# Kernel tuning notes

Measured on AMD Instinct MI355X. Metric: run time of the kernel, lower is better.

## Reference

```python
import jax, jax.numpy as jnp
import numpy as np

N = 50000      # nodes
E = 800000     # edges (before self loops)
IN = 128       # in_channels
HID = 64       # hidden_channels
HEADS = 4
NCLS = 2
NEG_SLOPE = 0.2
BN_EPS = 1e-5

# per-layer config: (in_dim, heads, out_c, concat)
LAYERS = [(IN, HEADS, HID, True), (HID*HEADS, HEADS, HID, True), (HID*HEADS, HEADS, HID, True), (HID*HEADS, 1, HID, False)]

def setup_inputs():
    key = jax.random.key(0)
    ks = iter(jax.random.split(key, 64))
    d = {}
    d['x'] = jax.random.normal(next(ks), (N, IN), dtype=jnp.float32)
    d['edge_index'] = jax.random.randint(next(ks), (2, E), 0, N, dtype=jnp.int64)
    for i, (inc, h, oc, concat) in enumerate(LAYERS):
        d[f'W{i}'] = jax.random.normal(next(ks), (inc, h*oc), dtype=jnp.float32) * (1.0/np.sqrt(inc))
        d[f'as{i}'] = jax.random.normal(next(ks), (h, oc), dtype=jnp.float32) * 0.1
        d[f'ad{i}'] = jax.random.normal(next(ks), (h, oc), dtype=jnp.float32) * 0.1
        bn_dim = h*oc if concat else oc
        d[f'b{i}'] = jnp.zeros((bn_dim,), dtype=jnp.float32)
        d[f'g{i}'] = jnp.ones((bn_dim,), dtype=jnp.float32)
        d[f'be{i}'] = jnp.zeros((bn_dim,), dtype=jnp.float32)
    d['hw1'] = jax.random.normal(next(ks), (HID, HID//2), dtype=jnp.float32) * (1.0/np.sqrt(HID))
    d['hb1'] = jnp.zeros((HID//2,), dtype=jnp.float32)
    d['hw2'] = jax.random.normal(next(ks), (HID//2, NCLS), dtype=jnp.float32) * (1.0/np.sqrt(HID//2))
    d['hb2'] = jnp.zeros((NCLS,), dtype=jnp.float32)
    return d

def _gat_layer(x, src, dst, W, a_src, a_dst, bias, heads, out_c, concat):
    n = x.shape[0]
    h = (x @ W).reshape(n, heads, out_c)                 # [N,H,C]
    asrc = jnp.einsum('nhc,hc->nh', h, a_src)            # [N,H]
    adst = jnp.einsum('nhc,hc->nh', h, a_dst)            # [N,H]
    e = asrc[src] + adst[dst]                            # [Etot,H]
    e = jax.nn.leaky_relu(e, NEG_SLOPE)
    # segment softmax over incoming edges of each dst node
    m = jax.ops.segment_max(e, dst, num_segments=n)
    m = jnp.where(jnp.isfinite(m), m, 0.0)
    ex = jnp.exp(e - m[dst])
    s = jax.ops.segment_sum(ex, dst, num_segments=n)
    alpha = ex / (s[dst] + 1e-16)                        # [Etot,H]
    msg = h[src] * alpha[:, :, None]                     # [Etot,H,C]
    out = jax.ops.segment_sum(msg, dst, num_segments=n)  # [N,H,C]
    out = out.reshape(n, heads*out_c) if concat else out.mean(axis=1)
    return out + bias

def _bn(x, g, b):
    mu = x.mean(axis=0)
    var = x.var(axis=0)
    return g * (x - mu) * jax.lax.rsqrt(var + BN_EPS) + b

def reference(x, edge_index,
              W0, as0, ad0, b0, g0, be0,
              W1, as1, ad1, b1, g1, be1,
              W2, as2, ad2, b2, g2, be2,
              W3, as3, ad3, b3, g3, be3,
              hw1, hb1, hw2, hb2):
    loop = jnp.arange(N, dtype=edge_index.dtype)
    src = jnp.concatenate([edge_index[0], loop])
    dst = jnp.concatenate([edge_index[1], loop])
    params = [(W0, as0, ad0, b0, g0, be0), (W1, as1, ad1, b1, g1, be1),
              (W2, as2, ad2, b2, g2, be2), (W3, as3, ad3, b3, g3, be3)]
    h = x
    for (inc, heads, oc, concat), (W, a_s, a_d, b, g, be) in zip(LAYERS, params):
        h = _gat_layer(h, src, dst, W, a_s, a_d, b, heads, oc, concat)
        h = _bn(h, g, be)
        h = jax.nn.relu(h)
    h = jax.nn.relu(h @ hw1 + hb1)
    return h @ hw2 + hb2
```

## Files before the change

### kernel.cpp

```cpp
#include <hip/hip_runtime.h>

typedef __attribute__((ext_vector_type(8))) short bf16x8;
typedef __attribute__((ext_vector_type(4))) float f32x4;

__device__ __forceinline__ float bf2f(unsigned short u) {
    union { unsigned int i; float f; } x;
    x.i = ((unsigned int)u) << 16;
    return x.f;
}
__device__ __forceinline__ unsigned short f2bf(float f) {
    union { float f; unsigned int i; } x;
    x.f = f;
    unsigned int r = x.i + 0x7fffu + ((x.i >> 16) & 1u);
    return (unsigned short)(r >> 16);
}
__device__ __forceinline__ float ldf(const void* p, int i, int f32m) {
    if (f32m) return ((const float*)p)[i];
    return bf2f(((const unsigned short*)p)[i]);
}
__device__ __forceinline__ void unpack2(unsigned int u, float& lo, float& hi) {
    union { unsigned int i; float f; } a, b;
    a.i = u << 16;
    b.i = u & 0xffff0000u;
    lo = a.f;
    hi = b.f;
}

__global__ void zero_kernel(int* p, int n) {
    int i = blockIdx.x * 256 + threadIdx.x;
    if (i < n) p[i] = 0;
}

__global__ void probe_kernel(const int* ei, const unsigned int* xw, int* meta) {
    if (threadIdx.x == 0 && blockIdx.x == 0) {
        int orv = 0;
        for (int k = 0; k < 64; k++) orv |= ei[2 * k + 1];
        meta[0] = (orv == 0) ? 1 : 0;
        int cnt = 0;
        for (int k = 0; k < 64; k++) {
            unsigned int w = xw[k];
            int e = (int)((w >> 23) & 0xffu);
            if (e >= 107 && e <= 140) cnt++;
        }
        meta[1] = (cnt >= 48) ? 1 : 0;
    }
}

__global__ void hist_kernel(const int* ei, const int* meta, int* cnt, int E, int N) {
    int e = blockIdx.x * 256 + threadIdx.x;
    if (e >= E) return;
    int d = meta[0] ? ei[2 * (E + e)] : ei[E + e];
    if ((unsigned)d >= (unsigned)N) d = 0;
    atomicAdd(&cnt[d], 1);
}

__global__ void __launch_bounds__(256) chunkred_kernel(const int* cnt, int* csum, int N) {
    __shared__ int red[256];
    int t = threadIdx.x;
    int idx = blockIdx.x * 256 + t;
    red[t] = (idx < N) ? cnt[idx] : 0;
    __syncthreads();
    for (int off = 128; off > 0; off >>= 1) {
        if (t < off) red[t] += red[t + off];
        __syncthreads();
    }
    if (t == 0) csum[blockIdx.x] = red[0];
}

__global__ void __launch_bounds__(256) scanc_kernel(const int* csum, int* cbase, int* offs,
                                                    int nch, int N) {
    __shared__ int part[256];
    int t = threadIdx.x;
    int v = (t < nch) ? csum[t] : 0;
    part[t] = v;
    __syncthreads();
    for (int off = 1; off < 256; off <<= 1) {
        int tv = (t >= off) ? part[t - off] : 0;
        __syncthreads();
        part[t] += tv;
        __syncthreads();
    }
    if (t < nch) cbase[t] = part[t] - v;
    if (t == nch - 1) offs[N] = part[t];
}

__global__ void __launch_bounds__(256) offs_kernel(const int* cnt, const int* cbase,
                                                   int* offs, int N) {
    __shared__ int part[256];
    int t = threadIdx.x;
    int idx = blockIdx.x * 256 + t;
    int v = (idx < N) ? cnt[idx] : 0;
    part[t] = v;
    __syncthreads();
    for (int off = 1; off < 256; off <<= 1) {
        int tv = (t >= off) ? part[t - off] : 0;
        __syncthreads();
        part[t] += tv;
        __syncthreads();
    }
    if (idx < N) offs[idx] = cbase[blockIdx.x] + part[t] - v;
}

__global__ void scatter_kernel(const int* ei, const int* meta, const int* offs,
                               int* fill, int* csr, int E, int N) {
    int e = blockIdx.x * 256 + threadIdx.x;
    if (e >= E) return;
    int is64 = meta[0];
    int sv = is64 ? ei[2 * e] : ei[e];
    int d  = is64 ? ei[2 * (E + e)] : ei[E + e];
    if ((unsigned)sv >= (unsigned)N) sv = 0;
    if ((unsigned)d  >= (unsigned)N) d  = 0;
    int pos = offs[d] + atomicAdd(&fill[d], 1);
    csr[pos] = sv;
}

__global__ void __launch_bounds__(256) split_kernel(const void* X, int x_is_input,
                                                    const int* meta, const float* scale,
                                                    const float* shift, int apply_bn,
                                                    unsigned short* hi, unsigned short* lo,
                                                    int total4, int kmask) {
    int idx = blockIdx.x * 256 + threadIdx.x;
    if (idx >= total4) return;
    int base = idx * 4;
    int xmode = x_is_input ? meta[1] : 1;
    float v[4];
    if (xmode) {
        float4 f = *(const float4*)((const float*)X + base);
        v[0] = f.x; v[1] = f.y; v[2] = f.z; v[3] = f.w;
    } else {
        uint2 u = *(const uint2*)((const unsigned short*)X + base);
        unpack2(u.x, v[0], v[1]);
        unpack2(u.y, v[2], v[3]);
    }
    if (apply_bn) {
        int f0 = base & kmask;
        #pragma unroll
        for (int j = 0; j < 4; j++)
            v[j] = fmaxf(fmaf(v[j], scale[f0 + j], shift[f0 + j]), 0.0f);
    }
    unsigned short h[4], l[4];
    #pragma unroll
    for (int j = 0; j < 4; j++) {
        h[j] = f2bf(v[j]);
        l[j] = f2bf(v[j] - bf2f(h[j]));
    }
    uint2 ho, loo;
    ho.x = (unsigned int)h[0] | ((unsigned int)h[1] << 16);
    ho.y = (unsigned int)h[2] | ((unsigned int)h[3] << 16);
    loo.x = (unsigned int)l[0] | ((unsigned int)l[1] << 16);
    loo.y = (unsigned int)l[2] | ((unsigned int)l[3] << 16);
    *(uint2*)(hi + base) = ho;
    *(uint2*)(lo + base) = loo;
}

__global__ void __launch_bounds__(256) wsplit_all(const void* W0, const void* W1,
                                                  const void* W2, const void* W3,
                                                  const int* meta,
                                                  unsigned short* h0, unsigned short* l0,
                                                  unsigned short* h1, unsigned short* l1,
                                                  unsigned short* h2, unsigned short* l2,
                                                  unsigned short* h3, unsigned short* l3) {
    int e = blockIdx.x * 256 + threadIdx.x;
    const void* W;
    unsigned short *hi, *lo;
    int K, shift, idx;
    if (e < 32768)       { W = W0; hi = h0; lo = l0; K = 128; shift = 8; idx = e; }
    else if (e < 98304)  { W = W1; hi = h1; lo = l1; K = 256; shift = 8; idx = e - 32768; }
    else if (e < 163840) { W = W2; hi = h2; lo = l2; K = 256; shift = 8; idx = e - 98304; }
    else if (e < 180224) { W = W3; hi = h3; lo = l3; K = 256; shift = 6; idx = e - 163840; }
    else return;
    int k = idx >> shift;
    int n = idx & ((1 << shift) - 1);
    float x = ldf(W, idx, meta[1]);
    unsigned short h = f2bf(x);
    hi[n * K + k] = h;
    lo[n * K + k] = f2bf(x - bf2f(h));
}

__global__ void __launch_bounds__(256) gemm_mfma(const unsigned short* Ahi,
                                                 const unsigned short* Alo,
                                                 const unsigned short* Bhi,
                                                 const unsigned short* Blo,
                                                 void* Cout, int out_bf16,
                                                 const void* aw_s, const void* aw_d,
                                                 float* asrc, float* adst,
                                                 int M, int K, int NC, const int* meta) {
    __shared__ unsigned short sAhi[64 * 40];
    __shared__ unsigned short sAlo[64 * 40];
    __shared__ unsigned short sBhi[64 * 40];
    __shared__ unsigned short sBlo[64 * 40];
    int wmode = meta[1];
    int t = threadIdx.x;
    int wid = t >> 6;
    int lane = t & 63;
    int row0 = blockIdx.x * 64;
    int col0 = blockIdx.y * 64;
    int H = NC >> 6;

    int ar = t >> 2;
    int ak = (t & 3) * 8;

    f32x4 acc[4];
    #pragma unroll
    for (int i = 0; i < 4; i++) acc[i] = (f32x4){0.0f, 0.0f, 0.0f, 0.0f};

    int m = lane & 15;
    int q = lane >> 4;

    for (int kt = 0; kt < K; kt += 32) {
        {
            int gr = row0 + ar;
            uint4 h4 = {0, 0, 0, 0}, l4 = {0, 0, 0, 0};
            if (gr < M) {
                h4 = *(const uint4*)(Ahi + (size_t)gr * K + kt + ak);
                l4 = *(const uint4*)(Alo + (size_t)gr * K + kt + ak);
            }
            *(uint4*)(sAhi + ar * 40 + ak) = h4;
            *(uint4*)(sAlo + ar * 40 + ak) = l4;
            uint4 bh4 = *(const uint4*)(Bhi + (size_t)(col0 + ar) * K + kt + ak);
            uint4 bl4 = *(const uint4*)(Blo + (size_t)(col0 + ar) * K + kt + ak);
            *(uint4*)(sBhi + ar * 40 + ak) = bh4;
            *(uint4*)(sBlo + ar * 40 + ak) = bl4;
        }
        __syncthreads();

        bf16x8 ahi = *(const bf16x8*)(sAhi + (wid * 16 + m) * 40 + q * 8);
        bf16x8 alo = *(const bf16x8*)(sAlo + (wid * 16 + m) * 40 + q * 8);
        #pragma unroll
        for (int tn = 0; tn < 4; tn++) {
            bf16x8 bhi = *(const bf16x8*)(sBhi + (tn * 16 + m) * 40 + q * 8);
            bf16x8 blo = *(const bf16x8*)(sBlo + (tn * 16 + m) * 40 + q * 8);
            acc[tn] = __builtin_amdgcn_mfma_f32_16x16x32_bf16(ahi, bhi, acc[tn], 0, 0, 0);
            acc[tn] = __builtin_amdgcn_mfma_f32_16x16x32_bf16(alo, bhi, acc[tn], 0, 0, 0);
            acc[tn] = __builtin_amdgcn_mfma_f32_16x16x32_bf16(ahi, blo, acc[tn], 0, 0, 0);
        }
        __syncthreads();
    }

    #pragma unroll
    for (int tn = 0; tn < 4; tn++) {
        int gcol = col0 + tn * 16 + m;
        #pragma unroll
        for (int reg = 0; reg < 4; reg++) {
            int grow = row0 + wid * 16 + q * 4 + reg;
            if (grow < M) {
                if (out_bf16)
                    ((unsigned short*)Cout)[(size_t)grow * NC + gcol] = f2bf(acc[tn][reg]);
                else
                    ((float*)Cout)[(size_t)grow * NC + gcol] = acc[tn][reg];
            }
        }
    }

    float ps[4] = {0.f, 0.f, 0.f, 0.f};
    float pd[4] = {0.f, 0.f, 0.f, 0.f};
    #pragma unroll
    for (int tn = 0; tn < 4; tn++) {
        float asv = ldf(aw_s, blockIdx.y * 64 + tn * 16 + m, wmode);
        float adv = ldf(aw_d, blockIdx.y * 64 + tn * 16 + m, wmode);
        #pragma unroll
        for (int reg = 0; reg < 4; reg++) {
            ps[reg] = fmaf(acc[tn][reg], asv, ps[reg]);
            pd[reg] = fmaf(acc[tn][reg], adv, pd[reg]);
        }
    }
    #pragma unroll
    for (int reg = 0; reg < 4; reg++) {
        #pragma unroll
        for (int off = 1; off < 16; off <<= 1) {
            ps[reg] += __shfl_xor(ps[reg], off);
            pd[reg] += __shfl_xor(pd[reg], off);
        }
    }
    if (m == 0) {
        #pragma unroll
        for (int reg = 0; reg < 4; reg++) {
            int grow = row0 + wid * 16 + q * 4 + reg;
            if (grow < M) {
                asrc[grow * H + blockIdx.y] = ps[reg];
                adst[grow * H + blockIdx.y] = pd[reg];
            }
        }
    }
}

__global__ void __launch_bounds__(256) aggb4(const unsigned short* hfb, const float* asrc,
                                             const float* adst, const int* offs,
                                             const int* csr, float* out, int N) {
    int wid = threadIdx.x >> 6;
    int l = threadIdx.x & 63;
    int node = blockIdx.x * 4 + wid;
    if (node >= N) return;
    int h = l >> 4;
    int beg = offs[node], end = offs[node + 1];
    float ad = adst[node * 4 + h];
    float e0 = asrc[node * 4 + h] + ad;
    e0 = (e0 < 0.0f) ? 0.2f * e0 : e0;
    float w0 = __expf(e0);
    uint2 u0 = ((const uint2*)(hfb + (size_t)node * 256))[l];
    float g0a, g0b, g0c, g0d;
    unpack2(u0.x, g0a, g0b);
    unpack2(u0.y, g0c, g0d);
    float s = w0;
    float a0 = w0 * g0a, a1 = w0 * g0b, a2 = w0 * g0c, a3 = w0 * g0d;
    int i = beg;
    for (; i + 4 <= end; i += 4) {
        int s0 = csr[i], s1 = csr[i + 1], s2 = csr[i + 2], s3 = csr[i + 3];
        float e_0 = asrc[s0 * 4 + h] + ad;
        float e_1 = asrc[s1 * 4 + h] + ad;
        float e_2 = asrc[s2 * 4 + h] + ad;
        float e_3 = asrc[s3 * 4 + h] + ad;
        uint2 u_0 = ((const uint2*)(hfb + (size_t)s0 * 256))[l];
        uint2 u_1 = ((const uint2*)(hfb + (size_t)s1 * 256))[l];
        uint2 u_2 = ((const uint2*)(hfb + (size_t)s2 * 256))[l];
        uint2 u_3 = ((const uint2*)(hfb + (size_t)s3 * 256))[l];
        e_0 = (e_0 < 0.0f) ? 0.2f * e_0 : e_0;
        e_1 = (e_1 < 0.0f) ? 0.2f * e_1 : e_1;
        e_2 = (e_2 < 0.0f) ? 0.2f * e_2 : e_2;
        e_3 = (e_3 < 0.0f) ? 0.2f * e_3 : e_3;
        float wv0 = __expf(e_0), wv1 = __expf(e_1), wv2 = __expf(e_2), wv3 = __expf(e_3);
        s += (wv0 + wv1) + (wv2 + wv3);
        float x0, x1, x2, x3;
        unpack2(u_0.x, x0, x1); unpack2(u_0.y, x2, x3);
        a0 = fmaf(wv0, x0, a0); a1 = fmaf(wv0, x1, a1);
        a2 = fmaf(wv0, x2, a2); a3 = fmaf(wv0, x3, a3);
        unpack2(u_1.x, x0, x1); unpack2(u_1.y, x2, x3);
        a0 = fmaf(wv1, x0, a0); a1 = fmaf(wv1, x1, a1);
        a2 = fmaf(wv1, x2, a2); a3 = fmaf(wv1, x3, a3);
        unpack2(u_2.x, x0, x1); unpack2(u_2.y, x2, x3);
        a0 = fmaf(wv2, x0, a0); a1 = fmaf(wv2, x1, a1);
        a2 = fmaf(wv2, x2, a2); a3 = fmaf(wv2, x3, a3);
        unpack2(u_3.x, x0, x1); unpack2(u_3.y, x2, x3);
        a0 = fmaf(wv3, x0, a0); a1 = fmaf(wv3, x1, a1);
        a2 = fmaf(wv3, x2, a2); a3 = fmaf(wv3, x3, a3);
    }
    for (; i < end; i++) {
        int sn = csr[i];
        float es = asrc[sn * 4 + h] + ad;
        es = (es < 0.0f) ? 0.2f * es : es;
        float wv = __expf(es);
        uint2 u = ((const uint2*)(hfb + (size_t)sn * 256))[l];
        float x0, x1, x2, x3;
        unpack2(u.x, x0, x1); unpack2(u.y, x2, x3);
        s += wv;
        a0 = fmaf(wv, x0, a0); a1 = fmaf(wv, x1, a1);
        a2 = fmaf(wv, x2, a2); a3 = fmaf(wv, x3, a3);
    }
    float rs = 1.0f / (s + 1e-16f);
    float4 o;
    o.x = a0 * rs; o.y = a1 * rs; o.z = a2 * rs; o.w = a3 * rs;
    *(float4*)&out[(size_t)node * 256 + l * 4] = o;
}

__global__ void __launch_bounds__(256) aggf1(const float* hf, const float* asrc,
                                             const float* adst, const int* offs,
                                             const int* csr, float* out, int N) {
    int wid = threadIdx.x >> 6;
    int c = threadIdx.x & 63;
    int node = blockIdx.x * 4 + wid;
    if (node >= N) return;
    int beg = offs[node], end = offs[node + 1];
    float ad = adst[node];
    float e0 = asrc[node] + ad;
    e0 = (e0 < 0.0f) ? 0.2f * e0 : e0;
    float w0 = __expf(e0);
    float s = w0;
    float acc0 = w0 * hf[(size_t)node * 64 + c];
    float acc1 = 0.0f, acc2 = 0.0f, acc3 = 0.0f;
    int i = beg;
    for (; i + 4 <= end; i += 4) {
        int s0 = csr[i], s1 = csr[i + 1], s2 = csr[i + 2], s3 = csr[i + 3];
        float e_0 = asrc[s0] + ad;
        float e_1 = asrc[s1] + ad;
        float e_2 = asrc[s2] + ad;
        float e_3 = asrc[s3] + ad;
        float g0 = hf[(size_t)s0 * 64 + c];
        float g1 = hf[(size_t)s1 * 64 + c];
        float g2 = hf[(size_t)s2 * 64 + c];
        float g3 = hf[(size_t)s3 * 64 + c];
        e_0 = (e_0 < 0.0f) ? 0.2f * e_0 : e_0;
        e_1 = (e_1 < 0.0f) ? 0.2f * e_1 : e_1;
        e_2 = (e_2 < 0.0f) ? 0.2f * e_2 : e_2;
        e_3 = (e_3 < 0.0f) ? 0.2f * e_3 : e_3;
        float w0_ = __expf(e_0), w1_ = __expf(e_1), w2_ = __expf(e_2), w3_ = __expf(e_3);
        s += (w0_ + w1_) + (w2_ + w3_);
        acc0 = fmaf(w0_, g0, acc0);
        acc1 = fmaf(w1_, g1, acc1);
        acc2 = fmaf(w2_, g2, acc2);
        acc3 = fmaf(w3_, g3, acc3);
    }
    for (; i < end; i++) {
        int sn = csr[i];
        float es = asrc[sn] + ad;
        es = (es < 0.0f) ? 0.2f * es : es;
        float wv = __expf(es);
        s += wv;
        acc0 = fmaf(wv, hf[(size_t)sn * 64 + c], acc0);
    }
    float acc = (acc0 + acc1) + (acc2 + acc3);
    out[(size_t)node * 64 + c] = acc / (s + 1e-16f);
}

__global__ void __launch_bounds__(256) bnstats_kernel(const float* x, float* partial,
                                                      int N, int NC, int c4shift) {
    __shared__ float4 ls[256];
    __shared__ float4 lq[256];
    int t = threadIdx.x;
    int c4 = t & ((1 << c4shift) - 1);
    int rsub = t >> c4shift;
    int rstep = 256 >> c4shift;
    int r0 = blockIdx.x * 256 + rsub;
    int r1 = blockIdx.x * 256 + 256;
    if (r1 > N) r1 = N;
    float4 s = {0.f, 0.f, 0.f, 0.f}, q = {0.f, 0.f, 0.f, 0.f};
    for (int r = r0; r < r1; r += rstep) {
        float4 v = *(const float4*)(x + (size_t)r * NC + c4 * 4);
        s.x += v.x; s.y += v.y; s.z += v.z; s.w += v.w;
        q.x = fmaf(v.x, v.x, q.x);
        q.y = fmaf(v.y, v.y, q.y);
        q.z = fmaf(v.z, v.z, q.z);
        q.w = fmaf(v.w, v.w, q.w);
    }
    ls[t] = s;
    lq[t] = q;
    __syncthreads();
    for (int step = 128; step >= (1 << c4shift); step >>= 1) {
        if (t < step) {
            float4 a = ls[t + step], b = lq[t + step];
            ls[t].x += a.x; ls[t].y += a.y; ls[t].z += a.z; ls[t].w += a.w;
            lq[t].x += b.x; lq[t].y += b.y; lq[t].z += b.z; lq[t].w += b.w;
        }
        __syncthreads();
    }
    if (t < (1 << c4shift)) {
        *(float4*)(partial + (size_t)blockIdx.x * 2 * NC + t * 4) = ls[t];
        *(float4*)(partial + (size_t)blockIdx.x * 2 * NC + NC + t * 4) = lq[t];
    }
}

__global__ void bnfinal(const float* partial, int nch, const void* g, const void* be,
                        float* scale, float* shift, int NC, float invN, const int* meta) {
    int f = threadIdx.x;
    if (f >= NC) return;
    int wmode = meta[1];
    float s = 0.0f, q = 0.0f;
    for (int b = 0; b < nch; b++) {
        s += partial[(size_t)b * 2 * NC + f];
        q += partial[(size_t)b * 2 * NC + NC + f];
    }
    float mu = s * invN;
    float var = q * invN - mu * mu;
    if (var < 0.0f) var = 0.0f;
    float rs = rsqrtf(var + 1e-5f);
    float sc = ldf(g, f, wmode) * rs;
    scale[f] = sc;
    shift[f] = ldf(be, f, wmode) - mu * sc;
}

__global__ void __launch_bounds__(256) head_kernel(const float* xin, const float* bnscale,
                                                   const float* bnshift, const void* hw1,
                                                   const void* hb1, const void* hw2,
                                                   const void* hb2, void* out, int N,
                                                   const int* meta) {
    __shared__ float w1[64 * 32];
    __shared__ float w2[64];
    __shared__ float b1[32];
    __shared__ float b2[2];
    __shared__ float sc[64];
    __shared__ float sh[64];
    int wmode = meta[1];
    for (int i = threadIdx.x; i < 2048; i += 256) w1[i] = ldf(hw1, i, wmode);
    if (threadIdx.x < 64) {
        w2[threadIdx.x] = ldf(hw2, threadIdx.x, wmode);
        sc[threadIdx.x] = bnscale[threadIdx.x];
        sh[threadIdx.x] = bnshift[threadIdx.x];
    }
    if (threadIdx.x < 32) b1[threadIdx.x] = ldf(hb1, threadIdx.x, wmode);
    if (threadIdx.x < 2) b2[threadIdx.x] = ldf(hb2, threadIdx.x, wmode);
    __syncthreads();
    int n = blockIdx.x * 256 + threadIdx.x;
    if (n >= N) return;
    float x[64];
    for (int i = 0; i < 64; i++)
        x[i] = fmaxf(fmaf(xin[(size_t)n * 64 + i], sc[i], sh[i]), 0.0f);
    float o0 = b2[0], o1 = b2[1];
    for (int j = 0; j < 32; j++) {
        float a = b1[j];
        #pragma unroll
        for (int k = 0; k < 64; k++) a = fmaf(x[k], w1[k * 32 + j], a);
        a = fmaxf(a, 0.0f);
        o0 = fmaf(a, w2[j * 2], o0);
        o1 = fmaf(a, w2[j * 2 + 1], o1);
    }
    if (wmode) {
        ((float*)out)[n * 2] = o0;
        ((float*)out)[n * 2 + 1] = o1;
    } else {
        ((unsigned short*)out)[n * 2] = f2bf(o0);
        ((unsigned short*)out)[n * 2 + 1] = f2bf(o1);
    }
}

extern "C" void kernel_launch(void* const* d_in, const int* in_sizes, int n_in,
                              void* d_out, int out_size, void* d_ws, size_t ws_size,
                              hipStream_t stream) {
    size_t out_bytes2 = (size_t)out_size * 2;

    if (n_in != 30 || in_sizes[0] != 50000 * 128 || in_sizes[1] != 2 * 800000 ||
        in_sizes[2] != 128 * 256 || in_sizes[26] != 64 * 32) {
        hipMemsetAsync(d_out, 0x4E, out_bytes2, stream);
        return;
    }

    const int N = 50000;
    const int E = 800000;

    const void* x_in = d_in[0];
    const int* ei = (const int*)d_in[1];
    const void* W0  = d_in[2];
    const void* As0 = d_in[3];
    const void* Ad0 = d_in[4];
    const void* G0  = d_in[6];
    const void* Be0 = d_in[7];
    const void* W1  = d_in[8];
    const void* As1 = d_in[9];
    const void* Ad1 = d_in[10];
    const void* G1  = d_in[12];
    const void* Be1 = d_in[13];
    const void* W2  = d_in[14];
    const void* As2 = d_in[15];
    const void* Ad2 = d_in[16];
    const void* G2  = d_in[18];
    const void* Be2 = d_in[19];
    const void* W3  = d_in[20];
    const void* As3 = d_in[21];
    const void* Ad3 = d_in[22];
    const void* G3  = d_in[24];
    const void* Be3 = d_in[25];
    const void* hw1 = d_in[26];
    const void* hb1 = d_in[27];
    const void* hw2 = d_in[28];
    const void* hb2 = d_in[29];

    char* base = (char*)d_ws;
    size_t off = 0;
    auto alloc = [&](size_t bytes) {
        void* r = (void*)(base + off);
        off += (bytes + 255) & ~(size_t)255;
        return r;
    };
    int nch = (N + 255) / 256;
    int* meta    = (int*)alloc(256);
    int* cnt     = (int*)alloc((size_t)N * 4);
    int* fill    = (int*)alloc((size_t)N * 4);
    size_t zero_end = off;
    float* partial = (float*)alloc((size_t)nch * 512 * 4);
    int* csum    = (int*)alloc(256 * 4);
    int* cbase   = (int*)alloc(256 * 4);
    int* offs    = (int*)alloc((size_t)(N + 1) * 4);
    int* csr     = (int*)alloc((size_t)E * 4);
    float* asrc  = (float*)alloc((size_t)N * 4 * 4);
    float* adst  = (float*)alloc((size_t)N * 4 * 4);
    float* scaleb = (float*)alloc(256 * 4);
    float* shiftb = (float*)alloc(256 * 4);
    unsigned short* hfb = (unsigned short*)alloc((size_t)N * 256 * 2);
    float* hff   = (float*)alloc((size_t)N * 64 * 4);
    float* xbuf  = (float*)alloc((size_t)N * 256 * 4);
    unsigned short* ahi = (unsigned short*)alloc((size_t)N * 256 * 2);
    unsigned short* alo = (unsigned short*)alloc((size_t)N * 256 * 2);
    unsigned short* w0hi = (unsigned short*)alloc(128 * 256 * 2);
    unsigned short* w0lo = (unsigned short*)alloc(128 * 256 * 2);
    unsigned short* w1hi = (unsigned short*)alloc(256 * 256 * 2);
    unsigned short* w1lo = (unsigned short*)alloc(256 * 256 * 2);
    unsigned short* w2hi = (unsigned short*)alloc(256 * 256 * 2);
    unsigned short* w2lo = (unsigned short*)alloc(256 * 256 * 2);
    unsigned short* w3hi = (unsigned short*)alloc(256 * 64 * 2);
    unsigned short* w3lo = (unsigned short*)alloc(256 * 64 * 2);

    if (ws_size < off) {
        hipMemsetAsync(d_out, 0x4D, out_bytes2, stream);
        return;
    }

    int zn = (int)((zero_end - 256) / 4);
    zero_kernel<<<(zn + 255) / 256, 256, 0, stream>>>(cnt, zn);
    probe_kernel<<<1, 64, 0, stream>>>(ei, (const unsigned int*)x_in, meta);

    int gE = (E + 255) / 256;
    hist_kernel<<<gE, 256, 0, stream>>>(ei, meta, cnt, E, N);
    chunkred_kernel<<<nch, 256, 0, stream>>>(cnt, csum, N);
    scanc_kernel<<<1, 256, 0, stream>>>(csum, cbase, offs, nch, N);
    offs_kernel<<<nch, 256, 0, stream>>>(cnt, cbase, offs, N);
    scatter_kernel<<<gE, 256, 0, stream>>>(ei, meta, offs, fill, csr, E, N);

    wsplit_all<<<(180224 + 255) / 256, 256, 0, stream>>>(
        W0, W1, W2, W3, meta, w0hi, w0lo, w1hi, w1lo, w2hi, w2lo, w3hi, w3lo);

    int gM64 = (N + 63) / 64;
    int gBN = nch;
    int gND = (N + 3) / 4;
    float invN = 1.0f / (float)N;

    const unsigned short* whi[4] = {w0hi, w1hi, w2hi, w3hi};
    const unsigned short* wlo[4] = {w0lo, w1lo, w2lo, w3lo};
    const void* Asl[4] = {As0, As1, As2, As3};
    const void* Adl[4] = {Ad0, Ad1, Ad2, Ad3};
    const void* Gl[4]  = {G0, G1, G2, G3};
    const void* Bel[4] = {Be0, Be1, Be2, Be3};

    for (int L = 0; L < 3; L++) {
        if (L == 0)
            split_kernel<<<(N * 128 / 4 + 255) / 256, 256, 0, stream>>>(
                x_in, 1, meta, scaleb, shiftb, 0, ahi, alo, N * 128 / 4, 127);
        else
            split_kernel<<<(N * 256 / 4 + 255) / 256, 256, 0, stream>>>(
                xbuf, 0, meta, scaleb, shiftb, 1, ahi, alo, N * 256 / 4, 255);
        int K = (L == 0) ? 128 : 256;
        gemm_mfma<<<dim3(gM64, 4), 256, 0, stream>>>(
            ahi, alo, whi[L], wlo[L], hfb, 1, Asl[L], Adl[L], asrc, adst, N, K, 256, meta);
        aggb4<<<gND, 256, 0, stream>>>(hfb, asrc, adst, offs, csr, xbuf, N);
        bnstats_kernel<<<gBN, 256, 0, stream>>>(xbuf, partial, N, 256, 6);
        bnfinal<<<1, 256, 0, stream>>>(partial, nch, Gl[L], Bel[L], scaleb, shiftb, 256, invN, meta);
    }

    split_kernel<<<(N * 256 / 4 + 255) / 256, 256, 0, stream>>>(
        xbuf, 0, meta, scaleb, shiftb, 1, ahi, alo, N * 256 / 4, 255);
    gemm_mfma<<<dim3(gM64, 1), 256, 0, stream>>>(
        ahi, alo, w3hi, w3lo, hff, 0, As3, Ad3, asrc, adst, N, 256, 64, meta);
    aggf1<<<gND, 256, 0, stream>>>(hff, asrc, adst, offs, csr, xbuf, N);
    bnstats_kernel<<<gBN, 256, 0, stream>>>(xbuf, partial, N, 64, 4);
    bnfinal<<<1, 256, 0, stream>>>(partial, nch, G3, Be3, scaleb, shiftb, 64, invN, meta);

    head_kernel<<<gBN, 256, 0, stream>>>(xbuf, scaleb, shiftb, hw1, hb1, hw2, hb2, d_out, N, meta);
}
```

Before: 954.9 us.

## Fuse BN-apply and bf16 hi/lo split into GEMM; parallelize BN statistics

Removes the standalone split kernel. The GEMM now loads fp32 activations directly, applies the previous layer's BN scale/shift and ReLU from shared memory, and splits each value into bf16 hi/lo before staging it in LDS. This drops a full write-and-read round trip of the activation matrix and its intermediate buffers on every layer. In exchange, the conversion is repeated for each column block of the GEMM. Separately, BN statistics now use 32-row blocks for more parallelism, and the final reduction is spread over several blocks with a shared-memory tree instead of one serial block.

After: 904.4 us. -5.3%, faster.

```diff
diff --git a/kernel.cpp b/kernel.cpp
--- a/kernel.cpp
+++ b/kernel.cpp
@@ -112,45 +112,6 @@
     if ((unsigned)d  >= (unsigned)N) d  = 0;
     int pos = offs[d] + atomicAdd(&fill[d], 1);
     csr[pos] = sv;
-}
-
-__global__ void __launch_bounds__(256) split_kernel(const void* X, int x_is_input,
-                                                    const int* meta, const float* scale,
-                                                    const float* shift, int apply_bn,
-                                                    unsigned short* hi, unsigned short* lo,
-                                                    int total4, int kmask) {
-    int idx = blockIdx.x * 256 + threadIdx.x;
-    if (idx >= total4) return;
-    int base = idx * 4;
-    int xmode = x_is_input ? meta[1] : 1;
-    float v[4];
-    if (xmode) {
-        float4 f = *(const float4*)((const float*)X + base);
-        v[0] = f.x; v[1] = f.y; v[2] = f.z; v[3] = f.w;
-    } else {
-        uint2 u = *(const uint2*)((const unsigned short*)X + base);
-        unpack2(u.x, v[0], v[1]);
-        unpack2(u.y, v[2], v[3]);
-    }
-    if (apply_bn) {
-        int f0 = base & kmask;
-        #pragma unroll
-        for (int j = 0; j < 4; j++)
-            v[j] = fmaxf(fmaf(v[j], scale[f0 + j], shift[f0 + j]), 0.0f);
-    }
-    unsigned short h[4], l[4];
-    #pragma unroll
-    for (int j = 0; j < 4; j++) {
-        h[j] = f2bf(v[j]);
-        l[j] = f2bf(v[j] - bf2f(h[j]));
-    }
-    uint2 ho, loo;
-    ho.x = (unsigned int)h[0] | ((unsigned int)h[1] << 16);
-    ho.y = (unsigned int)h[2] | ((unsigned int)h[3] << 16);
-    loo.x = (unsigned int)l[0] | ((unsigned int)l[1] << 16);
-    loo.y = (unsigned int)l[2] | ((unsigned int)l[3] << 16);
-    *(uint2*)(hi + base) = ho;
-    *(uint2*)(lo + base) = loo;
 }
 
 __global__ void __launch_bounds__(256) wsplit_all(const void* W0, const void* W1,
@@ -177,8 +138,9 @@
     lo[n * K + k] = f2bf(x - bf2f(h));
 }
 
-__global__ void __launch_bounds__(256) gemm_mfma(const unsigned short* Ahi,
-                                                 const unsigned short* Alo,
+__global__ void __launch_bounds__(256) gemm_mfma(const void* Aptr, int a_is_input,
+                                                 const float* bnscale, const float* bnshift,
+                                                 int apply_bn,
                                                  const unsigned short* Bhi,
                                                  const unsigned short* Blo,
                                                  void* Cout, int out_bf16,
@@ -189,7 +151,10 @@
     __shared__ unsigned short sAlo[64 * 40];
     __shared__ unsigned short sBhi[64 * 40];
     __shared__ unsigned short sBlo[64 * 40];
+    __shared__ float sScale[256];
+    __shared__ float sShift[256];
     int wmode = meta[1];
+    int amode = a_is_input ? wmode : 1;
     int t = threadIdx.x;
     int wid = t >> 6;
     int lane = t & 63;
@@ -197,6 +162,12 @@
     int col0 = blockIdx.y * 64;
     int H = NC >> 6;
 
+    if (apply_bn && t < K) {
+        sScale[t] = bnscale[t];
+        sShift[t] = bnshift[t];
+    }
+    __syncthreads();
+
     int ar = t >> 2;
     int ak = (t & 3) * 8;
 
@@ -210,13 +181,49 @@
     for (int kt = 0; kt < K; kt += 32) {
         {
             int gr = row0 + ar;
-            uint4 h4 = {0, 0, 0, 0}, l4 = {0, 0, 0, 0};
+            float v[8];
             if (gr < M) {
-                h4 = *(const uint4*)(Ahi + (size_t)gr * K + kt + ak);
-                l4 = *(const uint4*)(Alo + (size_t)gr * K + kt + ak);
+                if (amode) {
+                    const float* ap = (const float*)Aptr + (size_t)gr * K + kt + ak;
+                    float4 f0 = *(const float4*)ap;
+                    float4 f1 = *(const float4*)(ap + 4);
+                    v[0] = f0.x; v[1] = f0.y; v[2] = f0.z; v[3] = f0.w;
+                    v[4] = f1.x; v[5] = f1.y; v[6] = f1.z; v[7] = f1.w;
+                } else {
+                    const unsigned short* ap =
+                        (const unsigned short*)Aptr + (size_t)gr * K + kt + ak;
+                    uint4 u = *(const uint4*)ap;
+                    unpack2(u.x, v[0], v[1]);
+                    unpack2(u.y, v[2], v[3]);
+                    unpack2(u.z, v[4], v[5]);
+                    unpack2(u.w, v[6], v[7]);
+                }
+                if (apply_bn) {
+                    #pragma unroll
+                    for (int j = 0; j < 8; j++)
+                        v[j] = fmaxf(fmaf(v[j], sScale[kt + ak + j], sShift[kt + ak + j]), 0.0f);
+                }
+            } else {
+                #pragma unroll
+                for (int j = 0; j < 8; j++) v[j] = 0.0f;
             }
-            *(uint4*)(sAhi + ar * 40 + ak) = h4;
-            *(uint4*)(sAlo + ar * 40 + ak) = l4;
+            unsigned short h[8], l[8];
+            #pragma unroll
+            for (int j = 0; j < 8; j++) {
+                h[j] = f2bf(v[j]);
+                l[j] = f2bf(v[j] - bf2f(h[j]));
+            }
+            uint4 ho, lu;
+            ho.x = (unsigned int)h[0] | ((unsigned int)h[1] << 16);
+            ho.y = (unsigned int)h[2] | ((unsigned int)h[3] << 16);
+            ho.z = (unsigned int)h[4] | ((unsigned int)h[5] << 16);
+            ho.w = (unsigned int)h[6] | ((unsigned int)h[7] << 16);
+            lu.x = (unsigned int)l[0] | ((unsigned int)l[1] << 16);
+            lu.y = (unsigned int)l[2] | ((unsigned int)l[3] << 16);
+            lu.z = (unsigned int)l[4] | ((unsigned int)l[5] << 16);
+            lu.w = (unsigned int)l[6] | ((unsigned int)l[7] << 16);
+            *(uint4*)(sAhi + ar * 40 + ak) = ho;
+            *(uint4*)(sAlo + ar * 40 + ak) = lu;
             uint4 bh4 = *(const uint4*)(Bhi + (size_t)(col0 + ar) * K + kt + ak);
             uint4 bl4 = *(const uint4*)(Blo + (size_t)(col0 + ar) * K + kt + ak);
             *(uint4*)(sBhi + ar * 40 + ak) = bh4;
@@ -409,8 +416,8 @@
     int c4 = t & ((1 << c4shift) - 1);
     int rsub = t >> c4shift;
     int rstep = 256 >> c4shift;
-    int r0 = blockIdx.x * 256 + rsub;
-    int r1 = blockIdx.x * 256 + 256;
+    int r0 = blockIdx.x * 32 + rsub;
+    int r1 = blockIdx.x * 32 + 32;
     if (r1 > N) r1 = N;
     float4 s = {0.f, 0.f, 0.f, 0.f}, q = {0.f, 0.f, 0.f, 0.f};
     for (int r = r0; r < r1; r += rstep) {
@@ -438,23 +445,40 @@
     }
 }
 
-__global__ void bnfinal(const float* partial, int nch, const void* g, const void* be,
-                        float* scale, float* shift, int NC, float invN, const int* meta) {
-    int f = threadIdx.x;
-    if (f >= NC) return;
-    int wmode = meta[1];
+__global__ void __launch_bounds__(256) bnfinal(const float* partial, int nblk, const void* g,
+                                               const void* be, float* scale, float* shift,
+                                               int NC, float invN, const int* meta) {
+    __shared__ float rs_[256];
+    __shared__ float rq_[256];
+    int t = threadIdx.x;
+    int fl = t & 31;
+    int rg = t >> 5;
+    int f = blockIdx.x * 32 + fl;
     float s = 0.0f, q = 0.0f;
-    for (int b = 0; b < nch; b++) {
+    for (int b = rg; b < nblk; b += 8) {
         s += partial[(size_t)b * 2 * NC + f];
         q += partial[(size_t)b * 2 * NC + NC + f];
     }
-    float mu = s * invN;
-    float var = q * invN - mu * mu;
-    if (var < 0.0f) var = 0.0f;
-    float rs = rsqrtf(var + 1e-5f);
-    float sc = ldf(g, f, wmode) * rs;
-    scale[f] = sc;
-    shift[f] = ldf(be, f, wmode) - mu * sc;
+    rs_[t] = s;
+    rq_[t] = q;
+    __syncthreads();
+    for (int step = 128; step >= 32; step >>= 1) {
+        if (t < step) {
+            rs_[t] += rs_[t + step];
+            rq_[t] += rq_[t + step];
+        }
+        __syncthreads();
+    }
+    if (t < 32) {
+        int wmode = meta[1];
+        float mu = rs_[t] * invN;
+        float var = rq_[t] * invN - mu * mu;
+        if (var < 0.0f) var = 0.0f;
+        float rsq = rsqrtf(var + 1e-5f);
+        float sc = ldf(g, f, wmode) * rsq;
+        scale[f] = sc;
+        shift[f] = ldf(be, f, wmode) - mu * sc;
+    }
 }
 
 __global__ void __launch_bounds__(256) head_kernel(const float* xin, const float* bnscale,
@@ -550,11 +574,12 @@
         return r;
     };
     int nch = (N + 255) / 256;
+    int nblkBN = (N + 31) / 32;
     int* meta    = (int*)alloc(256);
     int* cnt     = (int*)alloc((size_t)N * 4);
     int* fill    = (int*)alloc((size_t)N * 4);
     size_t zero_end = off;
-    float* partial = (float*)alloc((size_t)nch * 512 * 4);
+    float* partial = (float*)alloc((size_t)nblkBN * 512 * 4);
     int* csum    = (int*)alloc(256 * 4);
     int* cbase   = (int*)alloc(256 * 4);
     int* offs    = (int*)alloc((size_t)(N + 1) * 4);
@@ -566,8 +591,6 @@
     unsigned short* hfb = (unsigned short*)alloc((size_t)N * 256 * 2);
     float* hff   = (float*)alloc((size_t)N * 64 * 4);
     float* xbuf  = (float*)alloc((size_t)N * 256 * 4);
-    unsigned short* ahi = (unsigned short*)alloc((size_t)N * 256 * 2);
-    unsigned short* alo = (unsigned short*)alloc((size_t)N * 256 * 2);
     unsigned short* w0hi = (unsigned short*)alloc(128 * 256 * 2);
     unsigned short* w0lo = (unsigned short*)alloc(128 * 256 * 2);
     unsigned short* w1hi = (unsigned short*)alloc(256 * 256 * 2);
@@ -597,7 +620,6 @@
         W0, W1, W2, W3, meta, w0hi, w0lo, w1hi, w1lo, w2hi, w2lo, w3hi, w3lo);
 
     int gM64 = (N + 63) / 64;
-    int gBN = nch;
     int gND = (N + 3) / 4;
     float invN = 1.0f / (float)N;
 
@@ -610,26 +632,26 @@
 
     for (int L = 0; L < 3; L++) {
         if (L == 0)
-            split_kernel<<<(N * 128 / 4 + 255) / 256, 256, 0, stream>>>(
-                x_in, 1, meta, scaleb, shiftb, 0, ahi, alo, N * 128 / 4, 127);
+            gemm_mfma<<<dim3(gM64, 4), 256, 0, stream>>>(
+                x_in, 1, scaleb, shiftb, 0, whi[L], wlo[L], hfb, 1,
+                Asl[L], Adl[L], asrc, adst, N, 128, 256, meta);
         else
-            split_kernel<<<(N * 256 / 4 + 255) / 256, 256, 0, stream>>>(
-                xbuf, 0, meta, scaleb, shiftb, 1, ahi, alo, N * 256 / 4, 255);
-        int K = (L == 0) ? 128 : 256;
-        gemm_mfma<<<dim3(gM64, 4), 256, 0, stream>>>(
-            ahi, alo, whi[L], wlo[L], hfb, 1, Asl[L], Adl[L], asrc, adst, N, K, 256, meta);
+            gemm_mfma<<<dim3(gM64, 4), 256, 0, stream>>>(
+                xbuf, 0, scaleb, shiftb, 1, whi[L], wlo[L], hfb, 1,
+                Asl[L], Adl[L], asrc, adst, N, 256, 256, meta);
         aggb4<<<gND, 256, 0, stream>>>(hfb, asrc, adst, offs, csr, xbuf, N);
-        bnstats_kernel<<<gBN, 256, 0, stream>>>(xbuf, partial, N, 256, 6);
-        bnfinal<<<1, 256, 0, stream>>>(partial, nch, Gl[L], Bel[L], scaleb, shiftb, 256, invN, meta);
-    }
-
-    split_kernel<<<(N * 256 / 4 + 255) / 256, 256, 0, stream>>>(
-        xbuf, 0, meta, scaleb, shiftb, 1, ahi, alo, N * 256 / 4, 255);
+        bnstats_kernel<<<nblkBN, 256, 0, stream>>>(xbuf, partial, N, 256, 6);
+        bnfinal<<<8, 256, 0, stream>>>(partial, nblkBN, Gl[L], Bel[L],
+                                       scaleb, shiftb, 256, invN, meta);
+    }
+
     gemm_mfma<<<dim3(gM64, 1), 256, 0, stream>>>(
-        ahi, alo, w3hi, w3lo, hff, 0, As3, Ad3, asrc, adst, N, 256, 64, meta);
+        xbuf, 0, scaleb, shiftb, 1, w3hi, w3lo, hff, 0,
+        As3, Ad3, asrc, adst, N, 256, 64, meta);
     aggf1<<<gND, 256, 0, stream>>>(hff, asrc, adst, offs, csr, xbuf, N);
-    bnstats_kernel<<<gBN, 256, 0, stream>>>(xbuf, partial, N, 64, 4);
-    bnfinal<<<1, 256, 0, stream>>>(partial, nch, G3, Be3, scaleb, shiftb, 64, invN, meta);
-
-    head_kernel<<<gBN, 256, 0, stream>>>(xbuf, scaleb, shiftb, hw1, hb1, hw2, hb2, d_out, N, meta);
-}
+    bnstats_kernel<<<nblkBN, 256, 0, stream>>>(xbuf, partial, N, 64, 4);
+    bnfinal<<<2, 256, 0, stream>>>(partial, nblkBN, G3, Be3, scaleb, shiftb, 64, invN, meta);
+
+    head_kernel<<<(N + 255) / 256, 256, 0, stream>>>(xbuf, scaleb, shiftb, hw1, hb1, hw2, hb2,
+                                                     d_out, N, meta);
+}
```
